# Performance work log

Hardware: AMD Instinct MI355X
Metric: run time of the kernel (lower is better)

Reference implementation:

```python
import jax, jax.numpy as jnp
import numpy as np

TWO_PI = np.float32(2.0 * np.pi)
N_GABORS = 256
H = W = 512


def setup_inputs() -> dict:
    key = jax.random.key(0)
    ks = jax.random.split(key, 10)
    f32 = jnp.float32
    return {
        "grid_x": jax.random.uniform(ks[0], (H, W), dtype=f32),
        "grid_y": jax.random.uniform(ks[1], (H, W), dtype=f32),
        "u": jax.random.normal(ks[2], (N_GABORS,), dtype=f32),
        "v": jax.random.normal(ks[3], (N_GABORS,), dtype=f32),
        "theta": 2.0 * jax.random.normal(ks[4], (N_GABORS,), dtype=f32),
        "rel_sigma": 0.05 + 0.7 * jax.random.normal(ks[5], (N_GABORS,), dtype=f32),
        "rel_freq": 0.03 + 5.0 * jax.random.normal(ks[6], (N_GABORS,), dtype=f32),
        "gamma": 0.03 + 0.15 * jax.random.normal(ks[7], (N_GABORS,), dtype=f32),
        "psi": 3.0 * jax.random.normal(ks[8], (N_GABORS, 3), dtype=f32),
        "amplitude": 0.2 * jax.random.normal(ks[9], (N_GABORS, 3), dtype=f32),
    }


def reference(grid_x, grid_y, u, v, theta, rel_sigma, rel_freq, gamma, psi, amplitude):
    # Parameter range enforcement (enforce_parameter_ranges + forward clamps)
    uc = jnp.clip(u, -1.0, 1.0)
    vc = jnp.clip(v, -1.0, 1.0)
    th = jnp.clip(theta, -2.0, 2.0) * TWO_PI           # [N]
    sig = jnp.clip(rel_sigma, 1e-5, 5.0)               # [N]
    gam = jnp.clip(gamma, 1e-5, 5.0)                   # [N]
    psi_c = jnp.clip(psi, -1.0, 1.0)                   # [N,3]
    amp = jnp.clip(amplitude, 0.0, 1.0)                # [N,3]

    cr = jnp.cos(th)[:, None, None]
    sr = jnp.sin(th)[:, None, None]
    dx = grid_x[None, :, :] - uc[:, None, None]        # [N,H,W]
    dy = grid_y[None, :, :] - vc[:, None, None]
    x_rot = dx * cr + dy * sr                          # [N,H,W]
    y_rot = -dx * sr + dy * cr

    gaussian = jnp.exp(jnp.clip(
        -x_rot ** 2 / (2.0 * sig[:, None, None] ** 2)
        - y_rot ** 2 / (2.0 * gam[:, None, None] ** 2),
        -80.0, 80.0))                                  # [N,H,W]

    freq = TWO_PI / jnp.exp(rel_freq)                  # [N]
    phase = psi_c * TWO_PI                             # [N,3]
    fx = freq[:, None, None] * x_rot                   # [N,H,W]

    # cos(fx + phase) = cos(fx)cos(phase) - sin(fx)sin(phase):
    # contract the gabor dim without materializing [N,3,H,W].
    gc = gaussian * jnp.cos(fx)                        # [N,H,W]
    gs = gaussian * jnp.sin(fx)                        # [N,H,W]
    result = (jnp.einsum('nhw,nc->chw', gc, amp * jnp.cos(phase))
              - jnp.einsum('nhw,nc->chw', gs, amp * jnp.sin(phase)))  # [3,H,W]
    return jnp.clip(result, -1.0, 1.0)
```

## Files before the change

### kernel.cpp

```cpp
#include <hip/hip_runtime.h>
#include <stdint.h>

#define NG 256
#define HW (512*512)
#define NCELL 1024
#define CAP 384
#define SPILL_CAP 4096
#define PXB 4096
#define TWO_PI_F 6.283185307179586f
#define L2E 1.4426950408889634f
#define INV2PI_D 0.15915494309189535

static __device__ __forceinline__ float clampf(float x, float lo, float hi) {
    return fminf(fmaxf(x, lo), hi);
}

static __device__ __forceinline__ void compute_consts(
    int n,
    const float* __restrict__ u, const float* __restrict__ v,
    const float* __restrict__ theta, const float* __restrict__ rel_sigma,
    const float* __restrict__ rel_freq, const float* __restrict__ gamma,
    const float* __restrict__ psi, const float* __restrict__ amplitude,
    float4& A, float4& B, float4& C, float4& D)
{
    const float uc = clampf(u[n], -1.f, 1.f);
    const float vc = clampf(v[n], -1.f, 1.f);
    const float th = clampf(theta[n], -2.f, 2.f) * TWO_PI_F;
    const float sg = clampf(rel_sigma[n], 1e-5f, 5.f);
    const float gm = clampf(gamma[n], 1e-5f, 5.f);
    const float cr = (float)::cos((double)th);
    const float sr = (float)::sin((double)th);
    const float i2s = 1.0f / (2.0f * sg * sg);
    const float i2g = 1.0f / (2.0f * gm * gm);
    const float E  = (float)::exp((double)rel_freq[n]);
    const float fq = TWO_PI_F / E;
    A = make_float4(uc, vc, cr, sr);
    B = make_float4(-(i2s * L2E), -(i2g * L2E), fq, 0.f);
    float ac[3], as[3];
    #pragma unroll
    for (int c = 0; c < 3; ++c) {
        const float ph = clampf(psi[n*3 + c], -1.f, 1.f) * TWO_PI_F;
        const float a  = clampf(amplitude[n*3 + c], 0.f, 1.f);
        ac[c] = a * (float)::cos((double)ph);
        as[c] = a * (float)::sin((double)ph);
    }
    C = make_float4(ac[0], ac[1], ac[2], 0.f);
    D = make_float4(as[0], as[1], as[2], 0.f);
}

static __device__ __forceinline__ void accum_list(
    const float4* __restrict__ base, int ngab,
    float gx, float gy, float& a0, float& a1, float& a2)
{
    const float c1f = 0.15915494309189535f;
    const float c2f = (float)(INV2PI_D - (double)0.15915494309189535f);
    for (int j = 0; j < ngab; ++j) {
        const float4 k0 = base[j];
        const float4 k1 = base[NG + j];
        const float dx = gx - k0.x;
        const float dy = gy - k0.y;
        float xr, yr;
        {
            #pragma clang fp contract(off)
            xr = dx * k0.z + dy * k0.w;
            yr = dy * k0.z - dx * k0.w;
        }
        const float e2 = fmaf(yr * yr, k1.y, xr * xr * k1.x);
        if (e2 > -20.0f) {
            const float g = __builtin_amdgcn_exp2f(e2);
            float fx;
            {
                #pragma clang fp contract(off)
                fx = k1.z * xr;
            }
            const float nn = __builtin_rintf(fx * c1f);
            float t = __builtin_fmaf(fx, c1f, -nn);
            t = __builtin_fmaf(fx, c2f, t);
            const float s = __builtin_amdgcn_sinf(t);
            const float c = __builtin_amdgcn_cosf(t);
            const float4 k2 = base[2*NG + j];
            const float4 k3 = base[3*NG + j];
            const float gc = g * c, gs = g * s;
            a0 = fmaf(gc, k2.x, fmaf(-gs, k3.x, a0));
            a1 = fmaf(gc, k2.y, fmaf(-gs, k3.y, a1));
            a2 = fmaf(gc, k2.z, fmaf(-gs, k3.z, a2));
        }
    }
}

__global__ __launch_bounds__(256) void gabor_bin_consts(
    const float* __restrict__ grid_x, const float* __restrict__ grid_y,
    const float* __restrict__ u, const float* __restrict__ v,
    const float* __restrict__ theta, const float* __restrict__ rel_sigma,
    const float* __restrict__ rel_freq, const float* __restrict__ gamma,
    const float* __restrict__ psi, const float* __restrict__ amplitude,
    float4* __restrict__ consts, int* __restrict__ counts,
    int* __restrict__ bucket, float2* __restrict__ bxy,
    int* __restrict__ spill, int* __restrict__ spilln)
{
    const int tid = threadIdx.x;
    if (blockIdx.x == 64) {
        float4 A, B, C, D;
        compute_consts(tid, u, v, theta, rel_sigma, rel_freq, gamma, psi,
                       amplitude, A, B, C, D);
        consts[tid] = A; consts[NG+tid] = B;
        consts[2*NG+tid] = C; consts[3*NG+tid] = D;
        return;
    }
    __shared__ int hist[NCELL];
    __shared__ int base[NCELL];
    #pragma unroll
    for (int i = 0; i < NCELL/256; ++i) hist[i*256 + tid] = 0;
    __syncthreads();

    uint32_t rec[PXB/256];
    const int p0 = blockIdx.x * PXB;
    #pragma unroll
    for (int i = 0; i < PXB/256; ++i) {
        const int p = p0 + i*256 + tid;
        const float x = grid_x[p], y = grid_y[p];
        int ix = (int)(x * 32.0f); ix = min(max(ix, 0), 31);
        int iy = (int)(y * 32.0f); iy = min(max(iy, 0), 31);
        const int cell = iy*32 + ix;
        const int lr = atomicAdd(&hist[cell], 1);
        rec[i] = ((uint32_t)cell << 13) | (uint32_t)lr;
    }
    __syncthreads();
    #pragma unroll
    for (int i = 0; i < NCELL/256; ++i) {
        const int c = i*256 + tid;
        const int h = hist[c];
        base[c] = (h > 0) ? atomicAdd(&counts[c], h) : 0;
    }
    __syncthreads();
    #pragma unroll
    for (int i = 0; i < PXB/256; ++i) {
        const int p = p0 + i*256 + tid;
        const int cell = (int)(rec[i] >> 13);
        const int g = base[cell] + (int)(rec[i] & 0x1FFFu);
        if (g < CAP) {
            bucket[cell*CAP + g] = p;
            bxy[cell*CAP + g] = make_float2(grid_x[p], grid_y[p]);
        } else {
            const int t2 = atomicAdd(spilln, 1);
            if (t2 < SPILL_CAP) spill[t2] = p;
        }
    }
}

__global__ __launch_bounds__(128) void gabor_render(
    const float4* __restrict__ consts, const int* __restrict__ counts,
    const int* __restrict__ bucket, const float2* __restrict__ bxy,
    const int* __restrict__ spill, const int* __restrict__ spilln,
    const float* __restrict__ grid_x, const float* __restrict__ grid_y,
    float* __restrict__ out)
{
    __shared__ float4 cs[4 * NG];
    __shared__ int s_wb[2];
    const int cell = blockIdx.x >> 1, par = blockIdx.x & 1;
    const int tid = threadIdx.x;
    const float cxc = ((cell & 31) + 0.5f) * 0.03125f;
    const float cyc = ((cell >> 5) + 0.5f) * 0.03125f;

    int total = 0;
    #pragma unroll
    for (int r = 0; r < 2; ++r) {
        const int g = r*128 + tid;
        const float4 A = consts[g];
        const float4 B = consts[NG + g];
        const float4 C = consts[2*NG + g];
        const float4 D = consts[3*NG + g];
        const float dx = cxc - A.x, dy = cyc - A.y;
        const float xrc = dx * A.z + dy * A.w;
        const float yrc = dy * A.z - dx * A.w;
        const float R = 0.0222f;
        const float xl = fmaxf(fabsf(xrc) - R, 0.f);
        const float yl = fmaxf(fabsf(yrc) - R, 0.f);
        const float e2max = xl*xl*B.x + yl*yl*B.y;
        const bool nz = (C.x != 0.f) | (C.y != 0.f) | (C.z != 0.f) |
                        (D.x != 0.f) | (D.y != 0.f) | (D.z != 0.f);
        const bool act = (e2max > -20.0f) && nz;
        const unsigned long long m = __ballot(act);
        const int lane = tid & 63, w = tid >> 6;
        if (lane == 0) s_wb[w] = __popcll(m);
        __syncthreads();
        const int pos = total + (w ? s_wb[0] : 0)
                      + __popcll(m & ((1ull << lane) - 1ull));
        if (act) { cs[pos] = A; cs[NG+pos] = B; cs[2*NG+pos] = C; cs[3*NG+pos] = D; }
        total += s_wb[0] + s_wb[1];
        __syncthreads();
    }
    const int ng = total;

    const float c1f = 0.15915494309189535f;
    const float c2f = (float)(INV2PI_D - (double)0.15915494309189535f);
    const int cnt = min(counts[cell], CAP);
    const int sb = cell * CAP;
    for (int i = par*128 + tid; i < cnt; i += 256) {
        const float2 xy = bxy[sb + i];
        float a0 = 0.f, a1 = 0.f, a2 = 0.f;
        #pragma unroll 2
        for (int j = 0; j < ng; ++j) {
            const float4 k0 = cs[j];
            const float4 k1 = cs[NG + j];
            const float dx = xy.x - k0.x;
            const float dy = xy.y - k0.y;
            float xr, yr;
            {
                #pragma clang fp contract(off)
                xr = dx * k0.z + dy * k0.w;
                yr = dy * k0.z - dx * k0.w;
            }
            const float e2 = fmaf(yr * yr, k1.y, xr * xr * k1.x);
            if (e2 > -20.0f) {
                const float g = __builtin_amdgcn_exp2f(e2);
                float fx;
                {
                    #pragma clang fp contract(off)
                    fx = k1.z * xr;
                }
                const float nn = __builtin_rintf(fx * c1f);
                float t = __builtin_fmaf(fx, c1f, -nn);
                t = __builtin_fmaf(fx, c2f, t);
                const float s = __builtin_amdgcn_sinf(t);
                const float c = __builtin_amdgcn_cosf(t);
                const float4 k2 = cs[2*NG + j];
                const float4 k3 = cs[3*NG + j];
                const float gc = g * c, gs = g * s;
                a0 = fmaf(gc, k2.x, fmaf(-gs, k3.x, a0));
                a1 = fmaf(gc, k2.y, fmaf(-gs, k3.y, a1));
                a2 = fmaf(gc, k2.z, fmaf(-gs, k3.z, a2));
            }
        }
        const int p = bucket[sb + i];
        out[p]        = clampf(a0, -1.f, 1.f);
        out[HW + p]   = clampf(a1, -1.f, 1.f);
        out[2*HW + p] = clampf(a2, -1.f, 1.f);
    }

    if (blockIdx.x == 0) {
        const int sc = min(*spilln, SPILL_CAP);
        for (int i = tid; i < sc; i += 128) {
            const int p = spill[i];
            const float gx = grid_x[p], gy = grid_y[p];
            float a0 = 0.f, a1 = 0.f, a2 = 0.f;
            accum_list(consts, NG, gx, gy, a0, a1, a2);
            out[p]        = clampf(a0, -1.f, 1.f);
            out[HW + p]   = clampf(a1, -1.f, 1.f);
            out[2*HW + p] = clampf(a2, -1.f, 1.f);
        }
    }
}

__global__ __launch_bounds__(256) void gabor_consts_kernel(
    const float* __restrict__ u, const float* __restrict__ v,
    const float* __restrict__ theta, const float* __restrict__ rel_sigma,
    const float* __restrict__ rel_freq, const float* __restrict__ gamma,
    const float* __restrict__ psi, const float* __restrict__ amplitude,
    float4* __restrict__ ws)
{
    const int n = threadIdx.x;
    float4 A, B, C, D;
    compute_consts(n, u, v, theta, rel_sigma, rel_freq, gamma, psi, amplitude,
                   A, B, C, D);
    ws[n] = A; ws[NG + n] = B; ws[2*NG + n] = C; ws[3*NG + n] = D;
}

__global__ __launch_bounds__(256) void gabor_fwd_ws(
    const float4* __restrict__ ws,
    const float* __restrict__ grid_x, const float* __restrict__ grid_y,
    float* __restrict__ out)
{
    __shared__ float4 cs[4 * NG];
    const int tid = threadIdx.x;
    cs[tid]        = ws[tid];
    cs[tid + NG]   = ws[tid + NG];
    cs[tid + 2*NG] = ws[tid + 2*NG];
    cs[tid + 3*NG] = ws[tid + 3*NG];
    __syncthreads();
    const int p = blockIdx.x * 256 + tid;
    const float gx = grid_x[p], gy = grid_y[p];
    float a0 = 0.f, a1 = 0.f, a2 = 0.f;
    accum_list(cs, NG, gx, gy, a0, a1, a2);
    out[p]        = clampf(a0, -1.f, 1.f);
    out[HW + p]   = clampf(a1, -1.f, 1.f);
    out[2*HW + p] = clampf(a2, -1.f, 1.f);
}

__global__ __launch_bounds__(256) void gabor_fwd_fused(
    const float* __restrict__ grid_x, const float* __restrict__ grid_y,
    const float* __restrict__ u, const float* __restrict__ v,
    const float* __restrict__ theta, const float* __restrict__ rel_sigma,
    const float* __restrict__ rel_freq, const float* __restrict__ gamma,
    const float* __restrict__ psi, const float* __restrict__ amplitude,
    float* __restrict__ out)
{
    __shared__ float4 cs[4 * NG];
    const int tid = threadIdx.x;
    {
        float4 A, B, C, D;
        compute_consts(tid, u, v, theta, rel_sigma, rel_freq, gamma, psi,
                       amplitude, A, B, C, D);
        cs[tid] = A; cs[tid + NG] = B; cs[tid + 2*NG] = C; cs[tid + 3*NG] = D;
    }
    __syncthreads();
    const int p = blockIdx.x * 256 + tid;
    const float gx = grid_x[p], gy = grid_y[p];
    float a0 = 0.f, a1 = 0.f, a2 = 0.f;
    accum_list(cs, NG, gx, gy, a0, a1, a2);
    out[p]        = clampf(a0, -1.f, 1.f);
    out[HW + p]   = clampf(a1, -1.f, 1.f);
    out[2*HW + p] = clampf(a2, -1.f, 1.f);
}

extern "C" void kernel_launch(void* const* d_in, const int* in_sizes, int n_in,
                              void* d_out, int out_size, void* d_ws, size_t ws_size,
                              hipStream_t stream) {
    const float* grid_x    = (const float*)d_in[0];
    const float* grid_y    = (const float*)d_in[1];
    const float* u         = (const float*)d_in[2];
    const float* v         = (const float*)d_in[3];
    const float* theta     = (const float*)d_in[4];
    const float* rel_sigma = (const float*)d_in[5];
    const float* rel_freq  = (const float*)d_in[6];
    const float* gamma     = (const float*)d_in[7];
    const float* psi       = (const float*)d_in[8];
    const float* amplitude = (const float*)d_in[9];
    float* out = (float*)d_out;

    const size_t OFF_CONSTS = 0;
    const size_t OFF_COUNTS = 16384;
    const size_t OFF_SPN    = 20480;
    const size_t OFF_SPILL  = 20736;
    const size_t OFF_BUCKET = 37120;
    const size_t OFF_BXY    = 1609984;
    const size_t NEED       = 4755712;

    char* w = (char*)d_ws;

    if (ws_size >= NEED) {
        float4* consts = (float4*)(w + OFF_CONSTS);
        int*    counts = (int*)(w + OFF_COUNTS);
        int*    spn    = (int*)(w + OFF_SPN);
        int*    spill  = (int*)(w + OFF_SPILL);
        int*    bucket = (int*)(w + OFF_BUCKET);
        float2* bxy    = (float2*)(w + OFF_BXY);

        hipMemsetAsync(w + OFF_COUNTS, 0, 4096 + 256, stream);
        gabor_bin_consts<<<65, 256, 0, stream>>>(
            grid_x, grid_y, u, v, theta, rel_sigma, rel_freq, gamma,
            psi, amplitude, consts, counts, bucket, bxy, spill, spn);
        gabor_render<<<2*NCELL, 128, 0, stream>>>(
            consts, counts, bucket, bxy, spill, spn, grid_x, grid_y, out);
    } else if (ws_size >= 4u * NG * sizeof(float4)) {
        float4* ws = (float4*)d_ws;
        gabor_consts_kernel<<<1, NG, 0, stream>>>(
            u, v, theta, rel_sigma, rel_freq, gamma, psi, amplitude, ws);
        gabor_fwd_ws<<<HW / 256, 256, 0, stream>>>(ws, grid_x, grid_y, out);
    } else {
        gabor_fwd_fused<<<HW / 256, 256, 0, stream>>>(
            grid_x, grid_y, u, v, theta, rel_sigma, rel_freq, gamma,
            psi, amplitude, out);
    }
}
```

Before: 38.96 us.

## Widen binning grid, pack pixel records, use one 256-thread render block per cell

The binning kernel now runs on 256 blocks of 1024 pixels instead of 64 blocks of 4096. It keeps each pixel's coordinates in registers and writes one packed float4 record (index, x, y) instead of separate bucket and xy arrays. The render kernel switches from two 128-thread blocks per cell to one 256-thread block per cell, so the gabor culling and shared-memory compaction run once per cell instead of twice. Trade-offs: packed records add 4 unused bytes per pixel, there are more global atomics on counts, and each cell's work now sits in a single larger block.

```diff
diff --git a/kernel.cpp b/kernel.cpp
--- a/kernel.cpp
+++ b/kernel.cpp
@@ -6,7 +6,8 @@
 #define NCELL 1024
 #define CAP 384
 #define SPILL_CAP 4096
-#define PXB 4096
+#define NBIN 256
+#define PXB (HW/NBIN)
 #define TWO_PI_F 6.283185307179586f
 #define L2E 1.4426950408889634f
 #define INV2PI_D 0.15915494309189535
@@ -95,11 +96,11 @@
     const float* __restrict__ rel_freq, const float* __restrict__ gamma,
     const float* __restrict__ psi, const float* __restrict__ amplitude,
     float4* __restrict__ consts, int* __restrict__ counts,
-    int* __restrict__ bucket, float2* __restrict__ bxy,
+    float4* __restrict__ bpx,
     int* __restrict__ spill, int* __restrict__ spilln)
 {
     const int tid = threadIdx.x;
-    if (blockIdx.x == 64) {
+    if (blockIdx.x == NBIN) {
         float4 A, B, C, D;
         compute_consts(tid, u, v, theta, rel_sigma, rel_freq, gamma, psi,
                        amplitude, A, B, C, D);
@@ -114,16 +115,18 @@
     __syncthreads();
 
     uint32_t rec[PXB/256];
+    float px[PXB/256], py[PXB/256];
     const int p0 = blockIdx.x * PXB;
     #pragma unroll
     for (int i = 0; i < PXB/256; ++i) {
         const int p = p0 + i*256 + tid;
         const float x = grid_x[p], y = grid_y[p];
+        px[i] = x; py[i] = y;
         int ix = (int)(x * 32.0f); ix = min(max(ix, 0), 31);
         int iy = (int)(y * 32.0f); iy = min(max(iy, 0), 31);
         const int cell = iy*32 + ix;
         const int lr = atomicAdd(&hist[cell], 1);
-        rec[i] = ((uint32_t)cell << 13) | (uint32_t)lr;
+        rec[i] = ((uint32_t)cell << 11) | (uint32_t)lr;
     }
     __syncthreads();
     #pragma unroll
@@ -136,11 +139,11 @@
     #pragma unroll
     for (int i = 0; i < PXB/256; ++i) {
         const int p = p0 + i*256 + tid;
-        const int cell = (int)(rec[i] >> 13);
-        const int g = base[cell] + (int)(rec[i] & 0x1FFFu);
+        const int cell = (int)(rec[i] >> 11);
+        const int g = base[cell] + (int)(rec[i] & 0x7FFu);
         if (g < CAP) {
-            bucket[cell*CAP + g] = p;
-            bxy[cell*CAP + g] = make_float2(grid_x[p], grid_y[p]);
+            bpx[cell*CAP + g] =
+                make_float4(__int_as_float(p), px[i], py[i], 0.f);
         } else {
             const int t2 = atomicAdd(spilln, 1);
             if (t2 < SPILL_CAP) spill[t2] = p;
@@ -148,28 +151,25 @@
     }
 }
 
-__global__ __launch_bounds__(128) void gabor_render(
+__global__ __launch_bounds__(256) void gabor_render(
     const float4* __restrict__ consts, const int* __restrict__ counts,
-    const int* __restrict__ bucket, const float2* __restrict__ bxy,
+    const float4* __restrict__ bpx,
     const int* __restrict__ spill, const int* __restrict__ spilln,
     const float* __restrict__ grid_x, const float* __restrict__ grid_y,
     float* __restrict__ out)
 {
     __shared__ float4 cs[4 * NG];
-    __shared__ int s_wb[2];
-    const int cell = blockIdx.x >> 1, par = blockIdx.x & 1;
+    __shared__ int s_wb[4];
+    const int cell = blockIdx.x;
     const int tid = threadIdx.x;
     const float cxc = ((cell & 31) + 0.5f) * 0.03125f;
     const float cyc = ((cell >> 5) + 0.5f) * 0.03125f;
 
-    int total = 0;
-    #pragma unroll
-    for (int r = 0; r < 2; ++r) {
-        const int g = r*128 + tid;
-        const float4 A = consts[g];
-        const float4 B = consts[NG + g];
-        const float4 C = consts[2*NG + g];
-        const float4 D = consts[3*NG + g];
+    {
+        const float4 A = consts[tid];
+        const float4 B = consts[NG + tid];
+        const float4 C = consts[2*NG + tid];
+        const float4 D = consts[3*NG + tid];
         const float dx = cxc - A.x, dy = cyc - A.y;
         const float xrc = dx * A.z + dy * A.w;
         const float yrc = dy * A.z - dx * A.w;
@@ -184,27 +184,32 @@
         const int lane = tid & 63, w = tid >> 6;
         if (lane == 0) s_wb[w] = __popcll(m);
         __syncthreads();
-        const int pos = total + (w ? s_wb[0] : 0)
-                      + __popcll(m & ((1ull << lane) - 1ull));
-        if (act) { cs[pos] = A; cs[NG+pos] = B; cs[2*NG+pos] = C; cs[3*NG+pos] = D; }
-        total += s_wb[0] + s_wb[1];
+        int base = 0;
+        #pragma unroll
+        for (int i = 0; i < 4; ++i) base += (i < w) ? s_wb[i] : 0;
+        if (act) {
+            const int pos = base + __popcll(m & ((1ull << lane) - 1ull));
+            cs[pos] = A; cs[NG+pos] = B; cs[2*NG+pos] = C; cs[3*NG+pos] = D;
+        }
         __syncthreads();
     }
-    const int ng = total;
+    const int ng = s_wb[0] + s_wb[1] + s_wb[2] + s_wb[3];
 
     const float c1f = 0.15915494309189535f;
     const float c2f = (float)(INV2PI_D - (double)0.15915494309189535f);
     const int cnt = min(counts[cell], CAP);
     const int sb = cell * CAP;
-    for (int i = par*128 + tid; i < cnt; i += 256) {
-        const float2 xy = bxy[sb + i];
+    for (int i = tid; i < cnt; i += 256) {
+        const float4 pxk = bpx[sb + i];
+        const int   p  = __float_as_int(pxk.x);
+        const float gx = pxk.y, gy = pxk.z;
         float a0 = 0.f, a1 = 0.f, a2 = 0.f;
         #pragma unroll 2
         for (int j = 0; j < ng; ++j) {
             const float4 k0 = cs[j];
             const float4 k1 = cs[NG + j];
-            const float dx = xy.x - k0.x;
-            const float dy = xy.y - k0.y;
+            const float dx = gx - k0.x;
+            const float dy = gy - k0.y;
             float xr, yr;
             {
                 #pragma clang fp contract(off)
@@ -232,15 +237,14 @@
                 a2 = fmaf(gc, k2.z, fmaf(-gs, k3.z, a2));
             }
         }
-        const int p = bucket[sb + i];
         out[p]        = clampf(a0, -1.f, 1.f);
         out[HW + p]   = clampf(a1, -1.f, 1.f);
         out[2*HW + p] = clampf(a2, -1.f, 1.f);
     }
 
-    if (blockIdx.x == 0) {
+    if (cell == 0) {
         const int sc = min(*spilln, SPILL_CAP);
-        for (int i = tid; i < sc; i += 128) {
+        for (int i = tid; i < sc; i += 256) {
             const int p = spill[i];
             const float gx = grid_x[p], gy = grid_y[p];
             float a0 = 0.f, a1 = 0.f, a2 = 0.f;
@@ -332,9 +336,8 @@
     const size_t OFF_COUNTS = 16384;
     const size_t OFF_SPN    = 20480;
     const size_t OFF_SPILL  = 20736;
-    const size_t OFF_BUCKET = 37120;
-    const size_t OFF_BXY    = 1609984;
-    const size_t NEED       = 4755712;
+    const size_t OFF_BPX    = 37120;
+    const size_t NEED       = 6328576;
 
     char* w = (char*)d_ws;
 
@@ -343,15 +346,14 @@
         int*    counts = (int*)(w + OFF_COUNTS);
         int*    spn    = (int*)(w + OFF_SPN);
         int*    spill  = (int*)(w + OFF_SPILL);
-        int*    bucket = (int*)(w + OFF_BUCKET);
-        float2* bxy    = (float2*)(w + OFF_BXY);
+        float4* bpx    = (float4*)(w + OFF_BPX);
 
         hipMemsetAsync(w + OFF_COUNTS, 0, 4096 + 256, stream);
-        gabor_bin_consts<<<65, 256, 0, stream>>>(
+        gabor_bin_consts<<<NBIN + 1, 256, 0, stream>>>(
             grid_x, grid_y, u, v, theta, rel_sigma, rel_freq, gamma,
-            psi, amplitude, consts, counts, bucket, bxy, spill, spn);
-        gabor_render<<<2*NCELL, 128, 0, stream>>>(
-            consts, counts, bucket, bxy, spill, spn, grid_x, grid_y, out);
+            psi, amplitude, consts, counts, bpx, spill, spn);
+        gabor_render<<<NCELL, 256, 0, stream>>>(
+            consts, counts, bpx, spill, spn, grid_x, grid_y, out);
     } else if (ws_size >= 4u * NG * sizeof(float4)) {
         float4* ws = (float4*)d_ws;
         gabor_consts_kernel<<<1, NG, 0, stream>>>(
```

Result: faster. 38.09 us (-2.2%).
